# Kernel optimization log

Measured on AMD Instinct MI355X. Metric: run time of the kernel, lower is better.

Reference implementation:

```python
import jax, jax.numpy as jnp
import numpy as np

N = 1024
NEVAL = 131072
NUM_POLES = 8
DOMAIN = (-1.0, 1.0)
DOMAIN_LEN = DOMAIN[1] - DOMAIN[0]
EPS = 1e-14


def _cheb_nodes(n):
    # Chebyshev points of the second kind: cos(pi * linspace(0, 1, n))
    return jnp.cos(jnp.pi * jnp.linspace(0.0, 1.0, n))


def _to_standard(x):
    return 2.0 * (x - DOMAIN[0]) / DOMAIN_LEN - 1.0


def _barycentric_weights(nodes, poles_real, poles_imag):
    # Vectorized equivalent of the original per-node Python loop.
    n = nodes.shape[0]
    diff = nodes[:, None] - nodes[None, :]            # (N, N)
    eye = jnp.eye(n, dtype=bool)
    # log_weights[j] = -sum_{i!=j} log|nodes[j]-nodes[i]|
    log_w = -jnp.sum(jnp.log(jnp.where(eye, 1.0, jnp.abs(diff))), axis=1)
    # signs[j] = (-1)^(# of negative off-diagonal diffs); diagonal diff==0 contributes nothing
    neg_count = jnp.sum(diff < 0, axis=1)
    signs = jnp.where(neg_count % 2 == 0, 1.0, -1.0)
    # each conjugate pole pair contributes 2*log(sqrt((x-r)^2 + i^2)) = log((x-r)^2 + i^2)
    pole_term = jnp.log((nodes[:, None] - poles_real[None, :]) ** 2
                        + poles_imag[None, :] ** 2)   # (N, M)
    log_w = log_w + jnp.sum(pole_term, axis=1)
    log_w = log_w - jnp.max(log_w)
    w = signs * jnp.exp(log_w)
    return w / jnp.abs(w[0])


def setup_inputs() -> dict:
    key = jax.random.key(0)
    k1, k2, k3, k4 = jax.random.split(key, 4)
    x_eval = jax.random.uniform(k1, (NEVAL,), dtype=jnp.float32)  # in [0,1) subset of domain
    values = jax.random.normal(k2, (N,), dtype=jnp.float32)
    poles_real = jax.random.normal(k3, (NUM_POLES,), dtype=jnp.float32)
    poles_imag = jax.random.normal(k4, (NUM_POLES,), dtype=jnp.float32)
    return {"x_eval": x_eval, "values": values,
            "poles_real": poles_real, "poles_imag": poles_imag}


def reference(x_eval, values, poles_real, poles_imag):
    nodes = _cheb_nodes(N)
    nodes_std = _to_standard(nodes)                   # identity for domain (-1,1)
    w = _barycentric_weights(nodes, poles_real, poles_imag)

    x_std = _to_standard(x_eval)
    d_x = x_std[None, :] - nodes_std[:, None]         # (N, NEVAL)
    small = jnp.abs(d_x) < EPS
    small_any = jnp.any(small, axis=0)                # (NEVAL,)
    d_safe = jnp.where(small, 1.0, d_x)
    inv = jnp.where(small_any[None, :], 0.0, 1.0 / d_safe)
    inv = jnp.where(small, 1.0, inv)                  # exact-hit columns: indicator row -> 1

    num = jnp.einsum('n,nm,n->m', values, inv, w)
    den = jnp.einsum('nm,n->m', inv, w)
    return num / den
```

## Files before the change

### kernel.cpp

```cpp
#include <hip/hip_runtime.h>
#include <math.h>

#define N_NODES 1024
#define N_EVAL 131072
#define NUM_POLES 8
#define PI_D 3.14159265358979323846


__global__ __launch_bounds__(256) void setup_kernel(
    const float* __restrict__ values,
    const float* __restrict__ poles_real,
    const float* __restrict__ poles_imag,
    float* __restrict__ ws) {
    const int j = blockIdx.x * 256 + threadIdx.x;
    const double nd = cos(PI_D * (double)j / (double)(N_NODES - 1));
    double prod = (j == 0 || j == N_NODES - 1) ? 0.5 : 1.0;
#pragma unroll
    for (int m = 0; m < NUM_POLES; ++m) {
        const double dr = nd - (double)poles_real[m];
        const double di = (double)poles_imag[m];
        prod *= dr * dr + di * di;
    }
    if (j & 1) prod = -prod;
    ws[j]        = (float)nd;
    ws[j + 1024] = (float)prod;
    ws[j + 2048] = (float)(prod * (double)values[j]);
}

__global__ __launch_bounds__(256, 8) void eval_scalar_kernel(
    const float* __restrict__ x_eval,
    const float* __restrict__ ws,
    float* __restrict__ out) {
    __shared__ float2 s_red[4][64];

    const int t = threadIdx.x;
    const int lane = t & 63;
    const int wid = __builtin_amdgcn_readfirstlane(t >> 6);
    const int pbase = blockIdx.x * 64;

    const float x = x_eval[pbase + lane];

    const float* __restrict__ nn = ws + wid * 256;
    const float* __restrict__ wq = ws + 1024 + wid * 256;
    const float* __restrict__ vq = ws + 2048 + wid * 256;

    float a0 = 0.0f, b0 = 0.0f, a1 = 0.0f, b1 = 0.0f;

#pragma unroll 2
    for (int j = 0; j < 256; j += 8) {
#pragma unroll
        for (int k = 0; k < 8; k += 2) {
            const float n0 = nn[j + k];
            const float w0 = wq[j + k];
            const float v0 = vq[j + k];
            const float n1 = nn[j + k + 1];
            const float w1 = wq[j + k + 1];
            const float v1 = vq[j + k + 1];
            const float d0 = x - n0;
            const float d1 = x - n1;
            const float r0 = __builtin_amdgcn_rcpf(d0);
            const float r1 = __builtin_amdgcn_rcpf(d1);
            a0 = fmaf(v0, r0, a0);
            b0 = fmaf(w0, r0, b0);
            a1 = fmaf(v1, r1, a1);
            b1 = fmaf(w1, r1, b1);
        }
    }

    s_red[wid][lane] = make_float2(a0 + a1, b0 + b1);
    __syncthreads();

    if (t < 64) {
        float num = 0.0f, den = 0.0f;
#pragma unroll
        for (int w = 0; w < 4; ++w) {
            const float2 p = s_red[w][t];
            num += p.x;
            den += p.y;
        }
        float res = num / den;
        if (__builtin_expect(__builtin_isnan(res), 0)) {
            const float xx = x_eval[pbase + t];
            float hn = 0.0f, hd = 0.0f;
            for (int jj = 0; jj < N_NODES; ++jj) {
                if (ws[jj] == xx) { hn += ws[2048 + jj]; hd += ws[1024 + jj]; }
            }
            res = hn / hd;
        }
        out[pbase + t] = res;
    }
}

__global__ __launch_bounds__(512, 4) void eval_kernel_fused(
    const float* __restrict__ x_eval,
    const float* __restrict__ values,
    const float* __restrict__ poles_real,
    const float* __restrict__ poles_imag,
    float* __restrict__ out) {
    __shared__ __align__(16) float s_n[N_NODES];
    __shared__ __align__(16) float s_w[N_NODES];
    __shared__ __align__(16) float s_v[N_NODES];
    __shared__ float2 s_r[8][256];

    const int t = threadIdx.x;

#pragma unroll
    for (int h = 0; h < 2; ++h) {
        const int j = t + h * 512;
        const double nd = cos(PI_D * (double)j / (double)(N_NODES - 1));
        double prod = (j == 0 || j == N_NODES - 1) ? 0.5 : 1.0;
#pragma unroll
        for (int m = 0; m < NUM_POLES; ++m) {
            const double dr = nd - (double)poles_real[m];
            const double di = (double)poles_imag[m];
            prod *= dr * dr + di * di;
        }
        if (j & 1) prod = -prod;
        s_n[j] = (float)nd;
        s_w[j] = (float)prod;
        s_v[j] = (float)(prod * (double)values[j]);
    }
    __syncthreads();

    const int lane = t & 63;
    const int wid  = t >> 6;
    const int pbase = blockIdx.x * 256;
    const float x0 = x_eval[pbase + lane];
    const float x1 = x_eval[pbase + 64 + lane];
    const float x2 = x_eval[pbase + 128 + lane];
    const float x3 = x_eval[pbase + 192 + lane];

    const float4* n4 = (const float4*)s_n + wid * 32;
    const float4* w4 = (const float4*)s_w + wid * 32;
    const float4* v4 = (const float4*)s_v + wid * 32;

    float a0 = 0.0f, b0 = 0.0f, a1 = 0.0f, b1 = 0.0f;
    float a2 = 0.0f, b2 = 0.0f, a3 = 0.0f, b3 = 0.0f;

#define NODE(C)                                                            \
    {                                                                      \
        const float d0 = x0 - an.C;                                        \
        const float d1 = x1 - an.C;                                        \
        const float d2 = x2 - an.C;                                        \
        const float d3 = x3 - an.C;                                        \
        const float r0 = __builtin_amdgcn_rcpf(d0);                        \
        const float r1 = __builtin_amdgcn_rcpf(d1);                        \
        const float r2 = __builtin_amdgcn_rcpf(d2);                        \
        const float r3 = __builtin_amdgcn_rcpf(d3);                        \
        a0 = fmaf(av.C, r0, a0); b0 = fmaf(aw.C, r0, b0);                  \
        a1 = fmaf(av.C, r1, a1); b1 = fmaf(aw.C, r1, b1);                  \
        a2 = fmaf(av.C, r2, a2); b2 = fmaf(aw.C, r2, b2);                  \
        a3 = fmaf(av.C, r3, a3); b3 = fmaf(aw.C, r3, b3);                  \
    }

#pragma unroll 4
    for (int q = 0; q < 32; ++q) {
        const float4 an = n4[q];
        const float4 aw = w4[q];
        const float4 av = v4[q];
        NODE(x) NODE(y) NODE(z) NODE(w)
    }
#undef NODE

    s_r[wid][lane]       = make_float2(a0, b0);
    s_r[wid][lane + 64]  = make_float2(a1, b1);
    s_r[wid][lane + 128] = make_float2(a2, b2);
    s_r[wid][lane + 192] = make_float2(a3, b3);
    __syncthreads();

    if (t < 256) {
        float nn = 0.0f, dd = 0.0f;
#pragma unroll
        for (int w = 0; w < 8; ++w) {
            const float2 pr = s_r[w][t];
            nn += pr.x;
            dd += pr.y;
        }
        float res = nn / dd;
        if (__builtin_expect(__builtin_isnan(res), 0)) {
            const float x = x_eval[pbase + t];
            float hn = 0.0f, hd = 0.0f;
            for (int j = 0; j < N_NODES; ++j) {
                if (s_n[j] == x) { hn += s_v[j]; hd += s_w[j]; }
            }
            res = hn / hd;
        }
        out[pbase + t] = res;
    }
}

extern "C" void kernel_launch(void* const* d_in, const int* in_sizes, int n_in,
                              void* d_out, int out_size, void* d_ws, size_t ws_size,
                              hipStream_t stream) {
    const float* x_eval     = (const float*)d_in[0];
    const float* values     = (const float*)d_in[1];
    const float* poles_real = (const float*)d_in[2];
    const float* poles_imag = (const float*)d_in[3];
    float* out = (float*)d_out;

    if (ws_size >= 3 * N_NODES * sizeof(float)) {
        float* ws = (float*)d_ws;
        setup_kernel<<<N_NODES / 256, 256, 0, stream>>>(values, poles_real,
                                                        poles_imag, ws);
        eval_scalar_kernel<<<N_EVAL / 64, 256, 0, stream>>>(x_eval, ws, out);
    } else {
        eval_kernel_fused<<<N_EVAL / 256, 512, 0, stream>>>(
            x_eval, values, poles_real, poles_imag, out);
    }
}
```

Measured before the change: 116.4 us.

## Combine node pairs into rational terms to halve reciprocals per evaluation

```diff
diff --git a/kernel.cpp b/kernel.cpp
--- a/kernel.cpp
+++ b/kernel.cpp
@@ -27,68 +27,71 @@
     ws[j + 2048] = (float)(prod * (double)values[j]);
 }
 
-__global__ __launch_bounds__(256, 8) void eval_scalar_kernel(
+__global__ __launch_bounds__(256) void setup_pairs_kernel(float* __restrict__ ws) {
+    const int k = blockIdx.x * 256 + threadIdx.x;
+    const double a   = (double)ws[2 * k];
+    const double b   = (double)ws[2 * k + 1];
+    const double w0  = (double)ws[1024 + 2 * k];
+    const double w1  = (double)ws[1024 + 2 * k + 1];
+    const double wv0 = (double)ws[2048 + 2 * k];
+    const double wv1 = (double)ws[2048 + 2 * k + 1];
+    float* p = ws + 3072 + k * 6;
+    p[0] = (float)(-a);
+    p[1] = (float)(-b);
+    p[2] = (float)(wv0 + wv1);
+    p[3] = (float)(-(wv0 * b + wv1 * a));
+    p[4] = (float)(w0 + w1);
+    p[5] = (float)(-(w0 * b + w1 * a));
+}
+
+__global__ __launch_bounds__(128) void eval_pairs_kernel(
     const float* __restrict__ x_eval,
     const float* __restrict__ ws,
     float* __restrict__ out) {
-    __shared__ float2 s_red[4][64];
-
     const int t = threadIdx.x;
     const int lane = t & 63;
-    const int wid = __builtin_amdgcn_readfirstlane(t >> 6);
-    const int pbase = blockIdx.x * 64;
+    const int wid  = __builtin_amdgcn_readfirstlane(t >> 6);
+    const int pbase = blockIdx.x * 128 + wid * 64;
 
     const float x = x_eval[pbase + lane];
-
-    const float* __restrict__ nn = ws + wid * 256;
-    const float* __restrict__ wq = ws + 1024 + wid * 256;
-    const float* __restrict__ vq = ws + 2048 + wid * 256;
+    const float* __restrict__ pt = ws + 3072;
 
     float a0 = 0.0f, b0 = 0.0f, a1 = 0.0f, b1 = 0.0f;
 
+#define PAIR(NA, NB, SV, TV, SW, TW, AA, BB)                                 \
+    {                                                                        \
+        const float d0 = x + (NA);                                           \
+        const float d1 = x + (NB);                                           \
+        const float q  = d0 * d1;                                            \
+        const float r  = __builtin_amdgcn_rcpf(q);                           \
+        const float nv = fmaf((SV), x, (TV));                                \
+        const float nw = fmaf((SW), x, (TW));                                \
+        AA = fmaf(nv, r, AA);                                                \
+        BB = fmaf(nw, r, BB);                                                \
+    }
+
 #pragma unroll 2
-    for (int j = 0; j < 256; j += 8) {
-#pragma unroll
-        for (int k = 0; k < 8; k += 2) {
-            const float n0 = nn[j + k];
-            const float w0 = wq[j + k];
-            const float v0 = vq[j + k];
-            const float n1 = nn[j + k + 1];
-            const float w1 = wq[j + k + 1];
-            const float v1 = vq[j + k + 1];
-            const float d0 = x - n0;
-            const float d1 = x - n1;
-            const float r0 = __builtin_amdgcn_rcpf(d0);
-            const float r1 = __builtin_amdgcn_rcpf(d1);
-            a0 = fmaf(v0, r0, a0);
-            b0 = fmaf(w0, r0, b0);
-            a1 = fmaf(v1, r1, a1);
-            b1 = fmaf(w1, r1, b1);
-        }
-    }
-
-    s_red[wid][lane] = make_float2(a0 + a1, b0 + b1);
-    __syncthreads();
-
-    if (t < 64) {
-        float num = 0.0f, den = 0.0f;
-#pragma unroll
-        for (int w = 0; w < 4; ++w) {
-            const float2 p = s_red[w][t];
-            num += p.x;
-            den += p.y;
-        }
-        float res = num / den;
-        if (__builtin_expect(__builtin_isnan(res), 0)) {
-            const float xx = x_eval[pbase + t];
-            float hn = 0.0f, hd = 0.0f;
-            for (int jj = 0; jj < N_NODES; ++jj) {
-                if (ws[jj] == xx) { hn += ws[2048 + jj]; hd += ws[1024 + jj]; }
-            }
-            res = hn / hd;
-        }
-        out[pbase + t] = res;
-    }
+    for (int k = 0; k < 512; k += 4) {
+        const float* c = pt + k * 6;
+        float C[24];
+#pragma unroll
+        for (int i = 0; i < 24; ++i) C[i] = c[i];
+        PAIR(C[0],  C[1],  C[2],  C[3],  C[4],  C[5],  a0, b0)
+        PAIR(C[6],  C[7],  C[8],  C[9],  C[10], C[11], a1, b1)
+        PAIR(C[12], C[13], C[14], C[15], C[16], C[17], a0, b0)
+        PAIR(C[18], C[19], C[20], C[21], C[22], C[23], a1, b1)
+    }
+#undef PAIR
+
+    float res = (a0 + a1) / (b0 + b1);
+    if (__builtin_expect(__builtin_isnan(res), 0)) {
+        float hn = 0.0f, hd = 0.0f;
+        for (int jj = 0; jj < N_NODES; ++jj) {
+            if (ws[jj] == x) { hn += ws[2048 + jj]; hd += ws[1024 + jj]; }
+        }
+        res = hn / hd;
+    }
+    out[pbase + lane] = res;
 }
 
 __global__ __launch_bounds__(512, 4) void eval_kernel_fused(
@@ -198,11 +201,12 @@
     const float* poles_imag = (const float*)d_in[3];
     float* out = (float*)d_out;
 
-    if (ws_size >= 3 * N_NODES * sizeof(float)) {
+    if (ws_size >= 6144 * sizeof(float)) {
         float* ws = (float*)d_ws;
         setup_kernel<<<N_NODES / 256, 256, 0, stream>>>(values, poles_real,
                                                         poles_imag, ws);
-        eval_scalar_kernel<<<N_EVAL / 64, 256, 0, stream>>>(x_eval, ws, out);
+        setup_pairs_kernel<<<2, 256, 0, stream>>>(ws);
+        eval_pairs_kernel<<<N_EVAL / 128, 128, 0, stream>>>(x_eval, ws, out);
     } else {
         eval_kernel_fused<<<N_EVAL / 256, 512, 0, stream>>>(
             x_eval, values, poles_real, poles_imag, out);
```

New measurement: 147.8 us. +27.0%, slower.
